# Kernel tuning notes

Hardware: AMD Instinct MI355X
Metric: run time of the kernel (lower is better)

Reference implementation:

```python
import jax, jax.numpy as jnp
import numpy as np
from jax import lax

B, L, D = 2, 1024, 1024
E = 2
DI = E * D            # d_inner = 2048
S = 16                # d_state
K = 4                 # d_conv
R = 64                # dt_rank = ceil(D/16)


def setup_inputs() -> dict:
    key = jax.random.key(0)
    ks = jax.random.split(key, 10)
    sc = 0.02
    inputs = jax.random.normal(ks[0], (B, L, D), dtype=jnp.float32)
    W_in = jax.random.normal(ks[1], (2 * DI, D), dtype=jnp.float32) * sc
    W_conv = jax.random.normal(ks[2], (DI, 1, K), dtype=jnp.float32) * sc  # depthwise (O,I/g,K)
    b_conv = jax.random.normal(ks[3], (DI,), dtype=jnp.float32) * sc
    W_x = jax.random.normal(ks[4], (R + 2 * S, DI), dtype=jnp.float32) * sc
    W_dt = jax.random.uniform(ks[5], (DI, R), dtype=jnp.float32, minval=-R ** -0.5, maxval=R ** -0.5)
    # dt bias = inverse-softplus of dt sampled log-uniform in [1e-3, 1e-1], as in the module init
    dt0 = jnp.exp(jax.random.uniform(ks[6], (DI,), dtype=jnp.float32) * (np.log(0.1) - np.log(0.001)) + np.log(0.001))
    dt0 = jnp.clip(dt0, 1e-4, None)
    b_dt = dt0 + jnp.log(-jnp.expm1(-dt0))
    A_log = jnp.log(jnp.tile(jnp.arange(1, S + 1, dtype=jnp.float32)[None, :], (DI, 1)))  # (DI, S)
    W_out = jax.random.normal(ks[7], (D, DI), dtype=jnp.float32) * sc
    return {"inputs": inputs, "W_in": W_in, "W_conv": W_conv, "b_conv": b_conv,
            "W_x": W_x, "W_dt": W_dt, "b_dt": b_dt, "A_log": A_log, "W_out": W_out}


def _selective_scan(u, dt, A, Bg, Cg):
    """h_t = exp(dt*A) h_{t-1} + dt*B_t*u_t ; y_t = C_t^T h_t.
    u,dt: (B,DI,L); A: (DI,S); Bg,Cg: (B,L,S). Returns (B,DI,L)."""
    batch = u.shape[0]
    d_inner, d_state = A.shape

    def step(state, xs):
        dt_t, B_t, C_t, u_t = xs                      # (B,DI),(B,S),(B,S),(B,DI)
        A_bar = jnp.exp(dt_t[..., None] * A)          # (B,DI,S)
        state = A_bar * state + dt_t[..., None] * B_t[:, None, :] * u_t[..., None]
        y = jnp.einsum('bcs,bs->bc', state, C_t)
        return state, y

    state0 = jnp.zeros((batch, d_inner, d_state), dtype=u.dtype)
    xs = (dt.transpose(2, 0, 1), Bg.transpose(1, 0, 2), Cg.transpose(1, 0, 2), u.transpose(2, 0, 1))
    _, ys = lax.scan(step, state0, xs)                # (L,B,DI)
    return ys.transpose(1, 2, 0)                      # (B,DI,L)


def reference(inputs, W_in, W_conv, b_conv, W_x, W_dt, b_dt, A_log, W_out):
    d_inner, _, k = W_conv.shape
    xz = inputs @ W_in.T                              # (B,L,2*DI)
    x, z = jnp.split(xz, 2, axis=-1)
    xc = x.transpose(0, 2, 1)                         # (B,DI,L)
    xc = jnp.pad(xc, ((0, 0), (0, 0), (k - 1, 0)))    # causal pad
    xc = lax.conv_general_dilated(xc, W_conv, window_strides=(1,), padding='VALID',
                                  dimension_numbers=('NCH', 'OIH', 'NCH'),
                                  feature_group_count=d_inner)
    xc = xc + b_conv[None, :, None]
    u = jax.nn.silu(xc)                               # (B,DI,L)
    feats = u.transpose(0, 2, 1)                      # (B,L,DI)
    proj = feats @ W_x.T                              # (B,L,R+2S)
    r = W_dt.shape[1]
    s = A_log.shape[1]
    dt_raw, Bg, Cg = proj[..., :r], proj[..., r:r + s], proj[..., r + s:]
    dt = jax.nn.softplus(dt_raw @ W_dt.T + b_dt)      # (B,L,DI)
    A = -jnp.exp(A_log)                               # (DI,S)
    y = _selective_scan(u, dt.transpose(0, 2, 1), A, Bg, Cg)  # (B,DI,L)
    gated = y * jax.nn.silu(z.transpose(0, 2, 1))     # (B,DI,L)
    return gated.transpose(0, 2, 1) @ W_out.T         # (B,L,D)
```

## Files before the change

kernel.cpp:

```cpp
#include <hip/hip_runtime.h>
#include <hip/hip_bf16.h>

#define BB 2
#define LL 1024
#define DD 1024
#define DI 2048
#define SS 16
#define KK 4
#define RR 64
#define MROWS (BB*LL)
#define NCT 32
#define CTL 32
#define PKZ 4

typedef __attribute__((ext_vector_type(8))) short short8;
typedef __attribute__((ext_vector_type(8))) _Float16 half8;
typedef __attribute__((ext_vector_type(4))) float floatx4;

__device__ __forceinline__ unsigned short f2h_bits(float v) {
    _Float16 h = (_Float16)v;
    return __builtin_bit_cast(unsigned short, h);
}

__device__ __forceinline__ void cast1_body(const float4* __restrict__ src,
                                           ushort4* __restrict__ d1,
                                           int i0, int stride, int n4) {
    for (int i = i0; i < n4; i += stride) {
        const float4 v = src[i];
        ushort4 o1;
        o1.x = f2h_bits(v.x); o1.y = f2h_bits(v.y);
        o1.z = f2h_bits(v.z); o1.w = f2h_bits(v.w);
        d1[i] = o1;
    }
}

__global__ __launch_bounds__(256) void cast3(
    const float4* __restrict__ s0, ushort4* __restrict__ d0, int n0, int nb0,
    const float4* __restrict__ s1, ushort4* __restrict__ d1, int n1, int nb1,
    const float4* __restrict__ s2, ushort4* __restrict__ d2, int n2) {
    const int bx = blockIdx.x;
    if (bx < nb0) {
        cast1_body(s0, d0, bx * 256 + threadIdx.x, nb0 * 256, n0);
    } else if (bx < nb0 + nb1) {
        cast1_body(s1, d1, (bx - nb0) * 256 + threadIdx.x, nb1 * 256, n1);
    } else {
        const int nb2 = gridDim.x - nb0 - nb1;
        cast1_body(s2, d2, (bx - nb0 - nb1) * 256 + threadIdx.x, nb2 * 256, n2);
    }
}

template <int NP>
__global__ __launch_bounds__(256, 2) void gemm_mfma_split(
    const unsigned short* __restrict__ A1, const unsigned short* __restrict__ A2,
    const unsigned short* __restrict__ B1, const unsigned short* __restrict__ B2,
    float* __restrict__ C0, float* __restrict__ Cpart,
    int M, int N, int Kstride, int Klen) {
    __shared__ unsigned short As[NP][8][128][8];
    __shared__ unsigned short Bs[NP][8][128][8];
    const int tid = threadIdx.x;
    const int bm = blockIdx.y * 128;
    const int bn = blockIdx.x * 128;
    const int Koff = blockIdx.z * Klen;
    float* __restrict__ C = (blockIdx.z == 0)
        ? C0 : (Cpart + (size_t)(blockIdx.z - 1) * M * N);

    const int lane = tid & 63;
    const int wv = tid >> 6;
    const int lm = lane & 15;
    const int kq = lane >> 4;
    const int wm = (wv >> 1) * 64;
    const int wn = (wv & 1) * 64;

    floatx4 acc[4][4];
    floatx4 acx[4][4];
    const floatx4 zf = {0.f, 0.f, 0.f, 0.f};
#pragma unroll
    for (int i = 0; i < 4; ++i)
#pragma unroll
        for (int j = 0; j < 4; ++j) { acc[i][j] = zf; acx[i][j] = zf; }

    const int r0 = tid >> 1;
    const int cc = tid & 1;
    const int cc0 = cc * 32;
    const int qb = cc * 4;

    const unsigned short* __restrict__ Ar1 = A1 + (size_t)(bm + r0) * Kstride;
    const unsigned short* __restrict__ Br1 = B1 + (size_t)(bn + r0) * Kstride;
    const unsigned short* __restrict__ Ar2 =
        (NP == 2) ? (A2 + (size_t)(bm + r0) * Kstride) : Ar1;
    const unsigned short* __restrict__ Br2 =
        (NP == 2) ? (B2 + (size_t)(bn + r0) * Kstride) : Br1;

    short8 pA[NP][4], pB[NP][4];
#define LOADK(kt)                                                        \
    {                                                                    \
        _Pragma("unroll")                                                \
        for (int j = 0; j < 4; ++j) {                                    \
            pA[0][j] = *(const short8*)&Ar1[(kt) + cc0 + j * 8];         \
            pB[0][j] = *(const short8*)&Br1[(kt) + cc0 + j * 8];         \
            if constexpr (NP == 2) {                                     \
                pA[1][j] = *(const short8*)&Ar2[(kt) + cc0 + j * 8];     \
                pB[1][j] = *(const short8*)&Br2[(kt) + cc0 + j * 8];     \
            }                                                            \
        }                                                                \
    }

#define PROD(p, bfq, ac)                                                                 \
        _Pragma("unroll")                                                                \
        for (int i = 0; i < 4; ++i)                                                      \
            _Pragma("unroll")                                                            \
            for (int j = 0; j < 4; ++j)                                                  \
                ac[i][j] = __builtin_amdgcn_mfma_f32_16x16x32_f16(af[p][i], bfq[j],      \
                                                                  ac[i][j], 0, 0, 0);

    LOADK(Koff)
    for (int kt = Koff; kt < Koff + Klen; kt += 64) {
#pragma unroll
        for (int p = 0; p < NP; ++p)
#pragma unroll
            for (int j = 0; j < 4; ++j) {
                *(short8*)&As[p][qb + j][r0][0] = pA[p][j];
                *(short8*)&Bs[p][qb + j][r0][0] = pB[p][j];
            }
        __syncthreads();

        const int ktn = (kt + 64 < Koff + Klen) ? (kt + 64) : Koff;
        LOADK(ktn)

#pragma unroll
        for (int ks = 0; ks < 2; ++ks) {
            const int q = ks * 4 + kq;
            half8 af[NP][4];
#pragma unroll
            for (int p = 0; p < NP; ++p)
#pragma unroll
                for (int i = 0; i < 4; ++i)
                    af[p][i] = *(const half8*)&As[p][q][wm + i * 16 + lm][0];

            {
                half8 bfq[4];
#pragma unroll
                for (int j = 0; j < 4; ++j)
                    bfq[j] = *(const half8*)&Bs[0][q][wn + j * 16 + lm][0];
                PROD(0, bfq, acc)
                if constexpr (NP == 2) { PROD(1, bfq, acx) }
            }
            if constexpr (NP == 2) {
                half8 bfq[4];
#pragma unroll
                for (int j = 0; j < 4; ++j)
                    bfq[j] = *(const half8*)&Bs[1][q][wn + j * 16 + lm][0];
                PROD(0, bfq, acx)
            }
        }
        __syncthreads();
    }
#undef PROD
#undef LOADK

    const float cs = 1.0f / 2048.0f;
#pragma unroll
    for (int i = 0; i < 4; ++i) {
        const int mrow = bm + wm + i * 16 + kq * 4;
#pragma unroll
        for (int j = 0; j < 4; ++j) {
            const int col = bn + wn + j * 16 + lm;
#pragma unroll
            for (int r = 0; r < 4; ++r) {
                float v = acc[i][j][r];
                if constexpr (NP == 2) v += cs * acx[i][j][r];
                C[(size_t)(mrow + r) * N + col] = v;
            }
        }
    }
}

__global__ __launch_bounds__(256) void reduce_add3(float4* __restrict__ dst,
                                                   const float4* __restrict__ src,
                                                   int n4) {
    for (int i = blockIdx.x * 256 + threadIdx.x; i < n4; i += gridDim.x * 256) {
        float4 a = dst[i];
        const float4 p0 = src[i];
        const float4 p1 = src[i + (size_t)n4];
        const float4 p2 = src[i + (size_t)2 * n4];
        a.x += p0.x + p1.x + p2.x;
        a.y += p0.y + p1.y + p2.y;
        a.z += p0.z + p1.z + p2.z;
        a.w += p0.w + p1.w + p2.w;
        dst[i] = a;
    }
}

__global__ __launch_bounds__(256) void conv_silu_rm8(const float* __restrict__ xz,
                                                     const float* __restrict__ Wc,
                                                     const float* __restrict__ bc,
                                                     float* __restrict__ u) {
    const int c = blockIdx.x * 256 + threadIdx.x;
    const int t0 = blockIdx.y * 8;
    const int b = blockIdx.z;
    const float* xcol = xz + (size_t)b * LL * (2 * DI) + c;
    const float w0 = Wc[c * 4 + 0], w1 = Wc[c * 4 + 1];
    const float w2 = Wc[c * 4 + 2], w3 = Wc[c * 4 + 3];
    const float bcv = bc[c];

    float x[11];
#pragma unroll
    for (int i = 0; i < 11; ++i) {
        const int t = t0 - 3 + i;
        x[i] = (t >= 0) ? xcol[(size_t)t * (2 * DI)] : 0.f;
    }
#pragma unroll
    for (int j = 0; j < 8; ++j) {
        const float acc = bcv + x[j] * w0 + x[j + 1] * w1 + x[j + 2] * w2 + x[j + 3] * w3;
        const size_t o = ((size_t)b * LL + t0 + j) * DI + c;
        u[o] = acc / (1.f + __expf(-acc));
    }
}

__global__ __launch_bounds__(256) void proj_gemm_sk(const float* __restrict__ U,
                                                    const float* __restrict__ Wx,
                                                    float* __restrict__ Pp) {
    const int BKp = 64;
    __shared__ float Us[16][68];
    __shared__ float Ws[96][68];
    const int tid = threadIdx.x;
    const int m0 = blockIdx.x * 16;
    const int Koff = blockIdx.y * (DI / PKZ);
    float* __restrict__ P = Pp + (size_t)blockIdx.y * MROWS * 96;
    const int tx = tid & 31;
    const int ty = tid >> 5;
    float acc[2][3] = {{0.f, 0.f, 0.f}, {0.f, 0.f, 0.f}};

    for (int kt = Koff; kt < Koff + DI / PKZ; kt += BKp) {
        {
            const int r = tid >> 4;
            const int c4 = (tid & 15) << 2;
            *(float4*)&Us[r][c4] = *(const float4*)&U[(size_t)(m0 + r) * DI + kt + c4];
        }
#pragma unroll
        for (int i = 0; i < 6; ++i) {
            const int idx = tid + i * 256;
            const int r = idx >> 4;
            const int c4 = (idx & 15) << 2;
            *(float4*)&Ws[r][c4] = *(const float4*)&Wx[(size_t)r * DI + kt + c4];
        }
        __syncthreads();
#pragma unroll
        for (int k4 = 0; k4 < BKp; k4 += 4) {
            const float4 u0 = *(const float4*)&Us[ty * 2][k4];
            const float4 u1 = *(const float4*)&Us[ty * 2 + 1][k4];
#pragma unroll
            for (int j = 0; j < 3; ++j) {
                const float4 w = *(const float4*)&Ws[tx + 32 * j][k4];
                acc[0][j] += u0.x * w.x + u0.y * w.y + u0.z * w.z + u0.w * w.w;
                acc[1][j] += u1.x * w.x + u1.y * w.y + u1.z * w.z + u1.w * w.w;
            }
        }
        __syncthreads();
    }
#pragma unroll
    for (int i = 0; i < 2; ++i)
#pragma unroll
        for (int j = 0; j < 3; ++j)
            P[(size_t)(m0 + ty * 2 + i) * 96 + tx + 32 * j] = acc[i][j];
}

__global__ __launch_bounds__(256) void proj_reduce(float4* __restrict__ P,
                                                   const float4* __restrict__ Pp,
                                                   int n4) {
    for (int i = blockIdx.x * 256 + threadIdx.x; i < n4; i += gridDim.x * 256) {
        const float4 a = Pp[i];
        const float4 b = Pp[i + (size_t)n4];
        const float4 c = Pp[i + (size_t)2 * n4];
        const float4 d = Pp[i + (size_t)3 * n4];
        P[i] = make_float4(a.x + b.x + c.x + d.x, a.y + b.y + c.y + d.y,
                           a.z + b.z + c.z + d.z, a.w + b.w + c.w + d.w);
    }
}

__global__ __launch_bounds__(256) void dt_gemm(const float* __restrict__ P,
                                               const float* __restrict__ Wdt,
                                               const float* __restrict__ bdt,
                                               float* __restrict__ dtb) {
    __shared__ float ps[16][68];
    const int tid = threadIdx.x;
    const int c = blockIdx.x * 256 + tid;
    const int m0 = blockIdx.y * 16;
    {
        const int r = tid >> 4;
        const int c4 = (tid & 15) << 2;
        *(float4*)&ps[r][c4] = *(const float4*)&P[(size_t)(m0 + r) * 96 + c4];
    }
    float w[64];
#pragma unroll
    for (int r4 = 0; r4 < 64; r4 += 4) {
        float4 v = *(const float4*)&Wdt[(size_t)c * 64 + r4];
        w[r4] = v.x; w[r4 + 1] = v.y; w[r4 + 2] = v.z; w[r4 + 3] = v.w;
    }
    const float bd = bdt[c];
    __syncthreads();
#pragma unroll 4
    for (int m = 0; m < 16; ++m) {
        float acc = bd;
#pragma unroll
        for (int r4 = 0; r4 < 64; r4 += 4) {
            float4 p = *(const float4*)&ps[m][r4];
            acc += p.x * w[r4] + p.y * w[r4 + 1] + p.z * w[r4 + 2] + p.w * w[r4 + 3];
        }
        const float sp = (acc > 20.f) ? acc : __logf(1.f + __expf(acc));
        dtb[(size_t)(m0 + m) * DI + c] = sp;
    }
}

__device__ __forceinline__ void pow_ladder(float e1, float ab[16]) {
    const float e2 = e1 * e1;
    const float e4 = e2 * e2;
    ab[0] = e1; ab[1] = e2; ab[2] = e2 * e1; ab[3] = e4;
#pragma unroll
    for (int s = 4; s < 16; ++s) ab[s] = ab[s - 4] * e4;
}

__global__ __launch_bounds__(256) void tscan1(const float* __restrict__ dtb,
                                              const float* __restrict__ u,
                                              const float* __restrict__ P,
                                              float* __restrict__ hend,
                                              float* __restrict__ sumdt) {
    const int c = blockIdx.x * 256 + threadIdx.x;
    const int ch = blockIdx.y;
    const int b = blockIdx.z;

    float h[16];
#pragma unroll
    for (int s = 0; s < 16; ++s) h[s] = 0.f;
    float sd = 0.f;

    const size_t m0 = (size_t)b * LL + (size_t)ch * CTL;
#pragma unroll 2
    for (int t = 0; t < CTL; ++t) {
        const size_t m = m0 + t;
        const float dt = dtb[m * DI + c];
        const float uv = u[m * DI + c];
        const float dtu = dt * uv;
        sd += dt;
        const float* __restrict__ bc = P + m * 96 + 64;
        float ab[16];
        pow_ladder(__expf(-dt), ab);
#pragma unroll
        for (int s = 0; s < 16; ++s) h[s] = ab[s] * h[s] + bc[s] * dtu;
    }
    const size_t o = (((size_t)b * NCT + ch) * DI + c) * 16;
#pragma unroll
    for (int s4 = 0; s4 < 16; s4 += 4)
        *(float4*)&hend[o + s4] = make_float4(h[s4], h[s4 + 1], h[s4 + 2], h[s4 + 3]);
    sumdt[((size_t)b * NCT + ch) * DI + c] = sd;
}

__global__ __launch_bounds__(256) void tscan2(float* __restrict__ hend,
                                              const float* __restrict__ sumdt) {
    const int id = blockIdx.x * 256 + threadIdx.x;
    const int s = id & 15;
    const int c = (id >> 4) & (DI - 1);
    const int b = id >> 15;
    const float Aval = -(float)(s + 1);
    float hs = 0.f;
#pragma unroll
    for (int g = 0; g < 4; ++g) {
        float he[8], sd[8];
#pragma unroll
        for (int j = 0; j < 8; ++j) {
            const size_t base = ((size_t)b * NCT + (g * 8 + j)) * DI + c;
            he[j] = hend[base * 16 + s];
            sd[j] = sumdt[base];
        }
#pragma unroll
        for (int j = 0; j < 8; ++j) {
            const size_t base = ((size_t)b * NCT + (g * 8 + j)) * DI + c;
            hend[base * 16 + s] = hs;
            hs = __expf(Aval * sd[j]) * hs + he[j];
        }
    }
}

__global__ __launch_bounds__(256) void tscan3(const float* __restrict__ dtb,
                                              const float* __restrict__ u,
                                              const float* __restrict__ P,
                                              const float* __restrict__ xz,
                                              const float* __restrict__ hstart,
                                              unsigned short* __restrict__ G1) {
    const int c = blockIdx.x * 256 + threadIdx.x;
    const int ch = blockIdx.y;
    const int b = blockIdx.z;

    float h[16];
    const size_t o = (((size_t)b * NCT + ch) * DI + c) * 16;
#pragma unroll
    for (int s4 = 0; s4 < 16; s4 += 4) {
        float4 v = *(const float4*)&hstart[o + s4];
        h[s4] = v.x; h[s4 + 1] = v.y; h[s4 + 2] = v.z; h[s4 + 3] = v.w;
    }

    const size_t m0 = (size_t)b * LL + (size_t)ch * CTL;
#pragma unroll 2
    for (int t = 0; t < CTL; ++t) {
        const size_t m = m0 + t;
        const float dt = dtb[m * DI + c];
        const float uv = u[m * DI + c];
        const float dtu = dt * uv;
        const float* __restrict__ bc = P + m * 96 + 64;
        float ab[16];
        pow_ladder(__expf(-dt), ab);
        float y = 0.f;
#pragma unroll
        for (int s = 0; s < 16; ++s) {
            h[s] = ab[s] * h[s] + bc[s] * dtu;
            y += bc[16 + s] * h[s];
        }
        const float zv = xz[m * (size_t)(2 * DI) + DI + c];
        const float g = y * (zv / (1.f + __expf(-zv)));
        G1[m * DI + c] = f2h_bits(g);
    }
}

extern "C" void kernel_launch(void* const* d_in, const int* in_sizes, int n_in,
                              void* d_out, int out_size, void* d_ws, size_t ws_size,
                              hipStream_t stream) {
    const float* inputs = (const float*)d_in[0];
    const float* W_in   = (const float*)d_in[1];
    const float* W_conv = (const float*)d_in[2];
    const float* b_conv = (const float*)d_in[3];
    const float* W_x    = (const float*)d_in[4];
    const float* W_dt   = (const float*)d_in[5];
    const float* b_dt   = (const float*)d_in[6];
    const float* W_out  = (const float*)d_in[8];
    float* out = (float*)d_out;

    float* ws = (float*)d_ws;
    float* xz      = ws;
    unsigned short* A1s = (unsigned short*)(ws + 8388608);
    unsigned short* B1s = (unsigned short*)(ws + 11534336);
    unsigned short* Wo1s = (unsigned short*)(ws + 14680064);
    float* u       = ws + 8388608;
    float* Pp      = ws + 12582912;
    float* sumdt   = ws + 16515072;
    float* P       = ws + 16777216;
    float* dtb     = ws + 16973824;
    unsigned short* G1s  = (unsigned short*)(ws + 12582912);
    float* hend    = out;
    float* P2p     = ws;

    cast3<<<3584, 256, 0, stream>>>(
        (const float4*)inputs, (ushort4*)A1s, 524288, 1024,
        (const float4*)W_in, (ushort4*)B1s, 1048576, 2048,
        (const float4*)W_out, (ushort4*)Wo1s, 524288);
    gemm_mfma_split<1><<<dim3(32, 16, 1), 256, 0, stream>>>(
        A1s, nullptr, B1s, nullptr, xz, xz, MROWS, 2 * DI, DD, DD);
    conv_silu_rm8<<<dim3(DI / 256, LL / 8, BB), 256, 0, stream>>>(xz, W_conv, b_conv, u);
    proj_gemm_sk<<<dim3(MROWS / 16, PKZ), 256, 0, stream>>>(u, W_x, Pp);
    proj_reduce<<<192, 256, 0, stream>>>((float4*)P, (const float4*)Pp, 49152);
    dt_gemm<<<dim3(DI / 256, MROWS / 16), 256, 0, stream>>>(P, W_dt, b_dt, dtb);
    tscan1<<<dim3(DI / 256, NCT, BB), 256, 0, stream>>>(dtb, u, P, hend, sumdt);
    tscan2<<<dim3(BB * DI * SS / 256), 256, 0, stream>>>(hend, sumdt);
    tscan3<<<dim3(DI / 256, NCT, BB), 256, 0, stream>>>(dtb, u, P, xz, hend, G1s);
    gemm_mfma_split<1><<<dim3(8, 16, 4), 256, 0, stream>>>(
        G1s, nullptr, Wo1s, nullptr, out, P2p, MROWS, DD, DI, DI / 4);
    reduce_add3<<<2048, 256, 0, stream>>>((float4*)out, (const float4*)P2p, 524288);
}
```

Measured before the change: 249.1 us.

## Store conv output as fp16 and run x-projection on MFMA with deeper split-K

The depthwise conv+SiLU output is now stored in fp16, which halves its write and the reads done by the projection and both scan kernels. The x-projection GEMM switches from an fp32 FMA kernel to an MFMA 16x16x32 fp16 kernel with register prefetch, using a pre-cast fp16 W_x and split-K raised to 16. This reduces memory traffic and ALU time in the projection, at the cost of fp16 rounding of u, a larger partial-sum buffer and a longer reduction. The Pp buffer now shares the dtb region, which is safe only because dtb is written after proj_reduce consumes Pp.

```diff
diff --git a/kernel.cpp b/kernel.cpp
--- a/kernel.cpp
+++ b/kernel.cpp
@@ -11,7 +11,7 @@
 #define MROWS (BB*LL)
 #define NCT 32
 #define CTL 32
-#define PKZ 4
+#define PKZ 16
 
 typedef __attribute__((ext_vector_type(8))) short short8;
 typedef __attribute__((ext_vector_type(8))) _Float16 half8;
@@ -20,6 +20,9 @@
 __device__ __forceinline__ unsigned short f2h_bits(float v) {
     _Float16 h = (_Float16)v;
     return __builtin_bit_cast(unsigned short, h);
+}
+__device__ __forceinline__ float h2f(unsigned short b) {
+    return (float)__builtin_bit_cast(_Float16, b);
 }
 
 __device__ __forceinline__ void cast1_body(const float4* __restrict__ src,
@@ -34,18 +37,21 @@
     }
 }
 
-__global__ __launch_bounds__(256) void cast3(
+__global__ __launch_bounds__(256) void cast4(
     const float4* __restrict__ s0, ushort4* __restrict__ d0, int n0, int nb0,
     const float4* __restrict__ s1, ushort4* __restrict__ d1, int n1, int nb1,
-    const float4* __restrict__ s2, ushort4* __restrict__ d2, int n2) {
+    const float4* __restrict__ s2, ushort4* __restrict__ d2, int n2, int nb2,
+    const float4* __restrict__ s3, ushort4* __restrict__ d3, int n3) {
     const int bx = blockIdx.x;
     if (bx < nb0) {
         cast1_body(s0, d0, bx * 256 + threadIdx.x, nb0 * 256, n0);
     } else if (bx < nb0 + nb1) {
         cast1_body(s1, d1, (bx - nb0) * 256 + threadIdx.x, nb1 * 256, n1);
+    } else if (bx < nb0 + nb1 + nb2) {
+        cast1_body(s2, d2, (bx - nb0 - nb1) * 256 + threadIdx.x, nb2 * 256, n2);
     } else {
-        const int nb2 = gridDim.x - nb0 - nb1;
-        cast1_body(s2, d2, (bx - nb0 - nb1) * 256 + threadIdx.x, nb2 * 256, n2);
+        const int nb3 = gridDim.x - nb0 - nb1 - nb2;
+        cast1_body(s3, d3, (bx - nb0 - nb1 - nb2) * 256 + threadIdx.x, nb3 * 256, n3);
     }
 }
 
@@ -194,7 +200,7 @@
 __global__ __launch_bounds__(256) void conv_silu_rm8(const float* __restrict__ xz,
                                                      const float* __restrict__ Wc,
                                                      const float* __restrict__ bc,
-                                                     float* __restrict__ u) {
+                                                     unsigned short* __restrict__ u16) {
     const int c = blockIdx.x * 256 + threadIdx.x;
     const int t0 = blockIdx.y * 8;
     const int b = blockIdx.z;
@@ -213,68 +219,92 @@
     for (int j = 0; j < 8; ++j) {
         const float acc = bcv + x[j] * w0 + x[j + 1] * w1 + x[j + 2] * w2 + x[j + 3] * w3;
         const size_t o = ((size_t)b * LL + t0 + j) * DI + c;
-        u[o] = acc / (1.f + __expf(-acc));
-    }
-}
-
-__global__ __launch_bounds__(256) void proj_gemm_sk(const float* __restrict__ U,
-                                                    const float* __restrict__ Wx,
-                                                    float* __restrict__ Pp) {
-    const int BKp = 64;
-    __shared__ float Us[16][68];
-    __shared__ float Ws[96][68];
+        u16[o] = f2h_bits(acc / (1.f + __expf(-acc)));
+    }
+}
+
+__global__ __launch_bounds__(256) void proj_mfma(const unsigned short* __restrict__ U16,
+                                                 const unsigned short* __restrict__ Wxs,
+                                                 float* __restrict__ Pp) {
+    __shared__ unsigned short As[8][64][8];
+    __shared__ unsigned short Bs[8][96][8];
     const int tid = threadIdx.x;
-    const int m0 = blockIdx.x * 16;
+    const int m0 = blockIdx.x * 64;
     const int Koff = blockIdx.y * (DI / PKZ);
     float* __restrict__ P = Pp + (size_t)blockIdx.y * MROWS * 96;
-    const int tx = tid & 31;
-    const int ty = tid >> 5;
-    float acc[2][3] = {{0.f, 0.f, 0.f}, {0.f, 0.f, 0.f}};
-
-    for (int kt = Koff; kt < Koff + DI / PKZ; kt += BKp) {
-        {
-            const int r = tid >> 4;
-            const int c4 = (tid & 15) << 2;
-            *(float4*)&Us[r][c4] = *(const float4*)&U[(size_t)(m0 + r) * DI + kt + c4];
-        }
-#pragma unroll
-        for (int i = 0; i < 6; ++i) {
-            const int idx = tid + i * 256;
-            const int r = idx >> 4;
-            const int c4 = (idx & 15) << 2;
-            *(float4*)&Ws[r][c4] = *(const float4*)&Wx[(size_t)r * DI + kt + c4];
+
+    const int lane = tid & 63;
+    const int wv = tid >> 6;
+    const int lm = lane & 15;
+    const int kq = lane >> 4;
+
+    floatx4 acc[6];
+    const floatx4 zf = {0.f, 0.f, 0.f, 0.f};
+#pragma unroll
+    for (int j = 0; j < 6; ++j) acc[j] = zf;
+
+    const int r0a = tid >> 2;
+    const int cca = tid & 3;
+    const unsigned short* __restrict__ Au = U16 + (size_t)(m0 + r0a) * DI;
+
+    short8 pA[2], pB[3];
+#define LOADKP(kt)                                                        \
+    {                                                                     \
+        pA[0] = *(const short8*)&Au[(kt) + cca * 16];                     \
+        pA[1] = *(const short8*)&Au[(kt) + cca * 16 + 8];                 \
+        _Pragma("unroll")                                                 \
+        for (int i = 0; i < 3; ++i) {                                     \
+            const int id = tid + i * 256;                                 \
+            pB[i] = *(const short8*)&Wxs[(size_t)(id >> 3) * DI + (kt) + (id & 7) * 8]; \
+        }                                                                 \
+    }
+
+    LOADKP(Koff)
+    for (int kt = Koff; kt < Koff + DI / PKZ; kt += 64) {
+        *(short8*)&As[cca * 2][r0a][0] = pA[0];
+        *(short8*)&As[cca * 2 + 1][r0a][0] = pA[1];
+#pragma unroll
+        for (int i = 0; i < 3; ++i) {
+            const int id = tid + i * 256;
+            *(short8*)&Bs[id & 7][id >> 3][0] = pB[i];
         }
         __syncthreads();
-#pragma unroll
-        for (int k4 = 0; k4 < BKp; k4 += 4) {
-            const float4 u0 = *(const float4*)&Us[ty * 2][k4];
-            const float4 u1 = *(const float4*)&Us[ty * 2 + 1][k4];
-#pragma unroll
-            for (int j = 0; j < 3; ++j) {
-                const float4 w = *(const float4*)&Ws[tx + 32 * j][k4];
-                acc[0][j] += u0.x * w.x + u0.y * w.y + u0.z * w.z + u0.w * w.w;
-                acc[1][j] += u1.x * w.x + u1.y * w.y + u1.z * w.z + u1.w * w.w;
+
+        const int ktn = (kt + 64 < Koff + DI / PKZ) ? (kt + 64) : Koff;
+        LOADKP(ktn)
+
+#pragma unroll
+        for (int ks = 0; ks < 2; ++ks) {
+            const int q = ks * 4 + kq;
+            const half8 af = *(const half8*)&As[q][wv * 16 + lm][0];
+#pragma unroll
+            for (int j = 0; j < 6; ++j) {
+                const half8 bf = *(const half8*)&Bs[q][j * 16 + lm][0];
+                acc[j] = __builtin_amdgcn_mfma_f32_16x16x32_f16(af, bf, acc[j], 0, 0, 0);
             }
         }
         __syncthreads();
     }
-#pragma unroll
-    for (int i = 0; i < 2; ++i)
-#pragma unroll
-        for (int j = 0; j < 3; ++j)
-            P[(size_t)(m0 + ty * 2 + i) * 96 + tx + 32 * j] = acc[i][j];
+#undef LOADKP
+
+#pragma unroll
+    for (int j = 0; j < 6; ++j)
+#pragma unroll
+        for (int r = 0; r < 4; ++r)
+            P[(size_t)(m0 + wv * 16 + kq * 4 + r) * 96 + j * 16 + lm] = acc[j][r];
 }
 
 __global__ __launch_bounds__(256) void proj_reduce(float4* __restrict__ P,
                                                    const float4* __restrict__ Pp,
                                                    int n4) {
     for (int i = blockIdx.x * 256 + threadIdx.x; i < n4; i += gridDim.x * 256) {
-        const float4 a = Pp[i];
-        const float4 b = Pp[i + (size_t)n4];
-        const float4 c = Pp[i + (size_t)2 * n4];
-        const float4 d = Pp[i + (size_t)3 * n4];
-        P[i] = make_float4(a.x + b.x + c.x + d.x, a.y + b.y + c.y + d.y,
-                           a.z + b.z + c.z + d.z, a.w + b.w + c.w + d.w);
+        float4 s = Pp[i];
+#pragma unroll
+        for (int z = 1; z < PKZ; ++z) {
+            const float4 v = Pp[i + (size_t)z * n4];
+            s.x += v.x; s.y += v.y; s.z += v.z; s.w += v.w;
+        }
+        P[i] = s;
     }
 }
 
@@ -321,7 +351,7 @@
 }
 
 __global__ __launch_bounds__(256) void tscan1(const float* __restrict__ dtb,
-                                              const float* __restrict__ u,
+                                              const unsigned short* __restrict__ u16,
                                               const float* __restrict__ P,
                                               float* __restrict__ hend,
                                               float* __restrict__ sumdt) {
@@ -339,7 +369,7 @@
     for (int t = 0; t < CTL; ++t) {
         const size_t m = m0 + t;
         const float dt = dtb[m * DI + c];
-        const float uv = u[m * DI + c];
+        const float uv = h2f(u16[m * DI + c]);
         const float dtu = dt * uv;
         sd += dt;
         const float* __restrict__ bc = P + m * 96 + 64;
@@ -382,7 +412,7 @@
 }
 
 __global__ __launch_bounds__(256) void tscan3(const float* __restrict__ dtb,
-                                              const float* __restrict__ u,
+                                              const unsigned short* __restrict__ u16,
                                               const float* __restrict__ P,
                                               const float* __restrict__ xz,
                                               const float* __restrict__ hstart,
@@ -404,7 +434,7 @@
     for (int t = 0; t < CTL; ++t) {
         const size_t m = m0 + t;
         const float dt = dtb[m * DI + c];
-        const float uv = u[m * DI + c];
+        const float uv = h2f(u16[m * DI + c]);
         const float dtu = dt * uv;
         const float* __restrict__ bc = P + m * 96 + 64;
         float ab[16];
@@ -439,8 +469,9 @@
     unsigned short* A1s = (unsigned short*)(ws + 8388608);
     unsigned short* B1s = (unsigned short*)(ws + 11534336);
     unsigned short* Wo1s = (unsigned short*)(ws + 14680064);
-    float* u       = ws + 8388608;
-    float* Pp      = ws + 12582912;
+    unsigned short* Wxs  = (unsigned short*)(ws + 15728640);
+    unsigned short* u16  = (unsigned short*)(ws + 8388608);
+    float* Pp      = ws + 16973824;
     float* sumdt   = ws + 16515072;
     float* P       = ws + 16777216;
     float* dtb     = ws + 16973824;
@@ -448,19 +479,20 @@
     float* hend    = out;
     float* P2p     = ws;
 
-    cast3<<<3584, 256, 0, stream>>>(
+    cast4<<<4288, 256, 0, stream>>>(
         (const float4*)inputs, (ushort4*)A1s, 524288, 1024,
         (const float4*)W_in, (ushort4*)B1s, 1048576, 2048,
-        (const float4*)W_out, (ushort4*)Wo1s, 524288);
+        (const float4*)W_out, (ushort4*)Wo1s, 524288, 1024,
+        (const float4*)W_x, (ushort4*)Wxs, 49152);
     gemm_mfma_split<1><<<dim3(32, 16, 1), 256, 0, stream>>>(
         A1s, nullptr, B1s, nullptr, xz, xz, MROWS, 2 * DI, DD, DD);
-    conv_silu_rm8<<<dim3(DI / 256, LL / 8, BB), 256, 0, stream>>>(xz, W_conv, b_conv, u);
-    proj_gemm_sk<<<dim3(MROWS / 16, PKZ), 256, 0, stream>>>(u, W_x, Pp);
+    conv_silu_rm8<<<dim3(DI / 256, LL / 8, BB), 256, 0, stream>>>(xz, W_conv, b_conv, u16);
+    proj_mfma<<<dim3(MROWS / 64, PKZ), 256, 0, stream>>>(u16, Wxs, Pp);
     proj_reduce<<<192, 256, 0, stream>>>((float4*)P, (const float4*)Pp, 49152);
     dt_gemm<<<dim3(DI / 256, MROWS / 16), 256, 0, stream>>>(P, W_dt, b_dt, dtb);
-    tscan1<<<dim3(DI / 256, NCT, BB), 256, 0, stream>>>(dtb, u, P, hend, sumdt);
+    tscan1<<<dim3(DI / 256, NCT, BB), 256, 0, stream>>>(dtb, u16, P, hend, sumdt);
     tscan2<<<dim3(BB * DI * SS / 256), 256, 0, stream>>>(hend, sumdt);
-    tscan3<<<dim3(DI / 256, NCT, BB), 256, 0, stream>>>(dtb, u, P, xz, hend, G1s);
+    tscan3<<<dim3(DI / 256, NCT, BB), 256, 0, stream>>>(dtb, u16, P, xz, hend, G1s);
     gemm_mfma_split<1><<<dim3(8, 16, 4), 256, 0, stream>>>(
         G1s, nullptr, Wo1s, nullptr, out, P2p, MROWS, DD, DI, DI / 4);
     reduce_add3<<<2048, 256, 0, stream>>>((float4*)out, (const float4*)P2p, 524288);
```

New measurement: 224.1 us (median of 3 runs). -10.1%, faster.
